# Kernel tuning notes

Hardware: AMD Instinct MI355X
Metric: run time of the kernel (lower is better)

## Reference

```python
import jax, jax.numpy as jnp
import numpy as np

B, T, D, H, F = 4, 2048, 512, 8, 2048
WINDOW = 128
HD = D // H
EPS = 1e-5


def layer_norm(x, g, b):
    mu = jnp.mean(x, axis=-1, keepdims=True)
    var = jnp.mean(jnp.square(x - mu), axis=-1, keepdims=True)
    return (x - mu) * jax.lax.rsqrt(var + EPS) * g + b


def setup_inputs() -> dict:
    key = jax.random.key(0)
    ks = jax.random.split(key, 5)
    s = 0.02
    return {
        "x": jax.random.normal(ks[0], (B, T, D), dtype=jnp.float32),
        "in_proj_w": jax.random.normal(ks[1], (3 * D, D), dtype=jnp.float32) * s,
        "in_proj_b": jnp.zeros((3 * D,), dtype=jnp.float32),
        "out_w": jax.random.normal(ks[2], (D, D), dtype=jnp.float32) * s,
        "out_b": jnp.zeros((D,), dtype=jnp.float32),
        "ln1_g": jnp.ones((D,), dtype=jnp.float32),
        "ln1_b": jnp.zeros((D,), dtype=jnp.float32),
        "ln2_g": jnp.ones((D,), dtype=jnp.float32),
        "ln2_b": jnp.zeros((D,), dtype=jnp.float32),
        "w1": jax.random.normal(ks[3], (F, D), dtype=jnp.float32) * s,
        "b1": jnp.zeros((F,), dtype=jnp.float32),
        "w2": jax.random.normal(ks[4], (D, F), dtype=jnp.float32) * s,
        "b2": jnp.zeros((D,), dtype=jnp.float32),
    }


def reference(x, in_proj_w, in_proj_b, out_w, out_b, ln1_g, ln1_b, ln2_g, ln2_b, w1, b1, w2, b2):
    # pre-norm sliding-window causal self-attention
    x2 = layer_norm(x, ln1_g, ln1_b)
    qkv = x2 @ in_proj_w.T + in_proj_b  # (B,T,3D)
    q, k, v = jnp.split(qkv, 3, axis=-1)
    q = q.reshape(B, T, H, HD)
    k = k.reshape(B, T, H, HD)
    v = v.reshape(B, T, H, HD)
    scale = 1.0 / np.sqrt(HD).astype(np.float32)
    scores = jnp.einsum("bthd,bshd->bhts", q, k) * scale  # dense (B,H,T,T)
    idx = jnp.arange(T)
    i = idx[:, None]
    j = idx[None, :]
    allowed = (j <= i) & (j >= i - WINDOW + 1)  # (T,T) bool, True = attend
    scores = jnp.where(allowed[None, None], scores, -jnp.inf)
    attn = jax.nn.softmax(scores, axis=-1)
    ctx = jnp.einsum("bhts,bshd->bthd", attn, v).reshape(B, T, D)
    attn_out = ctx @ out_w.T + out_b
    x = x + attn_out  # dropout is identity in eval
    # FFN block
    x3 = layer_norm(x, ln2_g, ln2_b)
    h = jax.nn.gelu(x3 @ w1.T + b1, approximate=False)
    x = x + h @ w2.T + b2
    return x
```

## Files before the change

### kernel.cpp

```cpp
#include <hip/hip_runtime.h>
#include <math.h>

constexpr int Bn = 4;
constexpr int Tn = 2048;
constexpr int Dn = 512;
constexpr int Hn = 8;
constexpr int HDn = 64;
constexpr int Fn = 2048;
constexpr int WIN = 128;
constexpr float EPS = 1e-5f;
constexpr int Mrows = Bn * Tn;
constexpr int QKVD = 3 * Dn;

using short8 = __attribute__((ext_vector_type(8))) short;
using f32x4  = __attribute__((ext_vector_type(4))) float;

__device__ __forceinline__ short f2bf(float f) {
    unsigned u = __float_as_uint(f);
    unsigned r = (u + 0x7FFFu + ((u >> 16) & 1u)) >> 16;
    return (short)r;
}

__device__ __forceinline__ float gelu_exact(float v) {
    return 0.5f * v * (1.0f + erff(v * 0.70710678118654752f));
}

__device__ __forceinline__ void async16(const short* g, short* l) {
    __builtin_amdgcn_global_load_lds(
        (const __attribute__((address_space(1))) void*)g,
        (__attribute__((address_space(3))) void*)l,
        16, 0, 0);
}

__global__ __launch_bounds__(256) void cvt_all(const float* __restrict__ s0,
                                               const float* __restrict__ s1,
                                               const float* __restrict__ s2,
                                               const float* __restrict__ s3,
                                               short* __restrict__ d0,
                                               short* __restrict__ d1,
                                               short* __restrict__ d2,
                                               short* __restrict__ d3)
{
    int i = blockIdx.x * 256 + threadIdx.x;
    const float* src; short* dst; int j;
    if (i < 196608)      { src = s0; dst = d0; j = i; }
    else if (i < 262144) { src = s1; dst = d1; j = i - 196608; }
    else if (i < 524288) { src = s2; dst = d2; j = i - 262144; }
    else                 { src = s3; dst = d3; j = i - 524288; }
    float4 v = ((const float4*)src)[j];
    short4 o;
    o.x = f2bf(v.x); o.y = f2bf(v.y); o.z = f2bf(v.z); o.w = f2bf(v.w);
    ((short4*)dst)[j] = o;
}

__global__ __launch_bounds__(64) void ln_kernel(const float* __restrict__ x,
                                                const float* __restrict__ g,
                                                const float* __restrict__ b,
                                                short* __restrict__ y)
{
    int row = blockIdx.x;
    int lane = threadIdx.x;
    const float4* xr = (const float4*)(x + (size_t)row * Dn);
    float4 v0 = xr[lane];
    float4 v1 = xr[lane + 64];
    float s = v0.x + v0.y + v0.z + v0.w + v1.x + v1.y + v1.z + v1.w;
#pragma unroll
    for (int off = 32; off >= 1; off >>= 1) s += __shfl_xor(s, off, 64);
    float mu = s * (1.0f / Dn);
    float d0x = v0.x - mu, d0y = v0.y - mu, d0z = v0.z - mu, d0w = v0.w - mu;
    float d1x = v1.x - mu, d1y = v1.y - mu, d1z = v1.z - mu, d1w = v1.w - mu;
    float q = d0x*d0x + d0y*d0y + d0z*d0z + d0w*d0w
            + d1x*d1x + d1y*d1y + d1z*d1z + d1w*d1w;
#pragma unroll
    for (int off = 32; off >= 1; off >>= 1) q += __shfl_xor(q, off, 64);
    float inv = rsqrtf(q * (1.0f / Dn) + EPS);
    const float4* gr = (const float4*)g;
    const float4* br = (const float4*)b;
    float4 g0 = gr[lane], g1 = gr[lane + 64];
    float4 b0 = br[lane], b1 = br[lane + 64];
    short4 a0, a1;
    a0.x = f2bf(d0x * inv * g0.x + b0.x);
    a0.y = f2bf(d0y * inv * g0.y + b0.y);
    a0.z = f2bf(d0z * inv * g0.z + b0.z);
    a0.w = f2bf(d0w * inv * g0.w + b0.w);
    a1.x = f2bf(d1x * inv * g1.x + b1.x);
    a1.y = f2bf(d1y * inv * g1.y + b1.y);
    a1.z = f2bf(d1z * inv * g1.z + b1.z);
    a1.w = f2bf(d1w * inv * g1.w + b1.w);
    short4* yr = (short4*)(y + (size_t)row * Dn);
    yr[lane] = a0;
    yr[lane + 64] = a1;
}

template <int MODE, int BK>
__global__ __launch_bounds__(256) void gemm_mfma(const short* __restrict__ A,
                                                 const short* __restrict__ Bw,
                                                 const float* __restrict__ bias,
                                                 const float* __restrict__ resid,
                                                 void* __restrict__ Cout,
                                                 short* __restrict__ q_out,
                                                 short* __restrict__ k_out,
                                                 short* __restrict__ v_out,
                                                 int M, int N, int K)
{
    constexpr int NCH = BK / 8;
    constexpr int LGN = (BK == 32) ? 2 : 3;
    constexpr int RPI = 512 / BK;
    constexpr int NI  = 32 / RPI;
    constexpr int BUF = 128 * BK;
    constexpr int KK  = BK / 32;
    __shared__ short SMEM[4 * BUF];
    short* Asb = SMEM;
    short* Bsb = SMEM + 2 * BUF;

    int tid = threadIdx.x;
    int w = tid >> 6, lane = tid & 63;
    int wr = w >> 1, wc = w & 1;
    int nN = N >> 7;
    int bid = blockIdx.x;
    int xcd = bid & 7, sq = bid >> 3;
    int mi = xcd + 8 * (sq / nN);
    int ni = sq % nN;
    int m0 = mi * 128, n0 = ni * 128;
    int quad = lane >> 4, l16 = lane & 15;

    f32x4 zero = {0.f, 0.f, 0.f, 0.f};
    f32x4 acc[4][4];
#pragma unroll
    for (int i = 0; i < 4; ++i)
#pragma unroll
        for (int j = 0; j < 4; ++j) acc[i][j] = zero;

    int rl = lane >> LGN;
    int ch = lane & (NCH - 1);
    const short* Ag[NI];
    const short* Bg[NI];
    int ldsOff[NI];
#pragma unroll
    for (int s = 0; s < NI; ++s) {
        int rowl = w * 32 + s * RPI + rl;
        int csw = (ch ^ ((rowl * BK >> 6) & (NCH - 1))) * 8;
        Ag[s] = A + (size_t)(m0 + rowl) * K + csw;
        Bg[s] = Bw + (size_t)(n0 + rowl) * K + csw;
        ldsOff[s] = (w * 32 + s * RPI) * BK;
    }

    auto stage = [&](int kt, int pp) {
#pragma unroll
        for (int s = 0; s < NI; ++s) {
            async16(Ag[s] + kt, Asb + pp * BUF + ldsOff[s]);
            async16(Bg[s] + kt, Bsb + pp * BUF + ldsOff[s]);
        }
    };

    stage(0, 0);
    int p = 0;
    for (int kt = 0; kt < K; kt += BK) {
        __syncthreads();
        if (kt + BK < K) stage(kt + BK, p ^ 1);
        short8 aF[KK][4], bF[KK][4];
#pragma unroll
        for (int kk = 0; kk < KK; ++kk)
#pragma unroll
            for (int i = 0; i < 4; ++i) {
                int ra = wr * 64 + i * 16 + l16;
                int rb = wc * 64 + i * 16 + l16;
                int cs = ((kk * 4 + quad) ^ ((ra * BK >> 6) & (NCH - 1))) * 8;
                aF[kk][i] = *(const short8*)(Asb + p * BUF + ra * BK + cs);
                bF[kk][i] = *(const short8*)(Bsb + p * BUF + rb * BK + cs);
            }
#pragma unroll
        for (int kk = 0; kk < KK; ++kk)
#pragma unroll
            for (int i = 0; i < 4; ++i)
#pragma unroll
                for (int j = 0; j < 4; ++j)
                    acc[i][j] = __builtin_amdgcn_mfma_f32_16x16x32_bf16(
                        aF[kk][i], bF[kk][j], acc[i][j], 0, 0, 0);
        p ^= 1;
    }

    if constexpr (MODE == 3) {
        __syncthreads();
        short* rp = SMEM + w * 2176;
        int b = m0 >> 11;
        int ncol0 = n0 + wc * 64;
        int sec = ncol0 >> 9;
        int h = (ncol0 & 511) >> 6;
        int bh = b * 8 + h;
        int t0 = (m0 & 2047) + wr * 64;
        if (sec == 2) {
#pragma unroll
            for (int ph = 0; ph < 2; ++ph) {
#pragma unroll
                for (int j = 2 * ph; j < 2 * ph + 2; ++j) {
                    int dl = (j - 2 * ph) * 16 + l16;
                    float bv = bias[ncol0 + j * 16 + l16];
#pragma unroll
                    for (int i = 0; i < 4; ++i)
#pragma unroll
                        for (int r = 0; r < 4; ++r)
                            rp[dl * 68 + i * 16 + quad * 4 + r] = f2bf(acc[i][j][r] + bv);
                }
#pragma unroll
                for (int it = 0; it < 4; ++it) {
                    int row = it * 8 + (lane >> 3);
                    int off = (lane & 7) * 8;
                    *(short8*)(v_out + ((size_t)bh * 64 + 32 * ph + row) * 2048 + t0 + off) =
                        *(const short8*)(rp + row * 68 + off);
                }
            }
        } else {
            short* dst = (sec == 0 ? q_out : k_out);
#pragma unroll
            for (int ph = 0; ph < 2; ++ph) {
#pragma unroll
                for (int i = 2 * ph; i < 2 * ph + 2; ++i) {
                    int tl = (i - 2 * ph) * 16 + quad * 4;
#pragma unroll
                    for (int j = 0; j < 4; ++j) {
                        float bv = bias[ncol0 + j * 16 + l16];
#pragma unroll
                        for (int r = 0; r < 4; ++r)
                            rp[(tl + r) * 68 + j * 16 + l16] = f2bf(acc[i][j][r] + bv);
                    }
                }
#pragma unroll
                for (int it = 0; it < 4; ++it) {
                    int row = it * 8 + (lane >> 3);
                    int off = (lane & 7) * 8;
                    *(short8*)(dst + ((size_t)bh * 2048 + t0 + 32 * ph + row) * 64 + off) =
                        *(const short8*)(rp + row * 68 + off);
                }
            }
        }
        return;
    }

    if constexpr (MODE == 2) {
        __syncthreads();
        short* rp = SMEM + w * 2176;
        short* Cb = (short*)Cout;
#pragma unroll
        for (int ph = 0; ph < 2; ++ph) {
#pragma unroll
            for (int i = 2 * ph; i < 2 * ph + 2; ++i) {
                int ml = (i - 2 * ph) * 16 + quad * 4;
#pragma unroll
                for (int j = 0; j < 4; ++j) {
                    float bv = bias[n0 + wc * 64 + j * 16 + l16];
#pragma unroll
                    for (int r = 0; r < 4; ++r)
                        rp[(ml + r) * 68 + j * 16 + l16] =
                            f2bf(gelu_exact(acc[i][j][r] + bv));
                }
            }
#pragma unroll
            for (int it = 0; it < 4; ++it) {
                int row = it * 8 + (lane >> 3);
                int off = (lane & 7) * 8;
                *(short8*)(Cb + (size_t)(m0 + wr * 64 + 32 * ph + row) * N
                              + n0 + wc * 64 + off) =
                    *(const short8*)(rp + row * 68 + off);
            }
        }
        return;
    }

    float* Cf = (float*)Cout;
#pragma unroll
    for (int j = 0; j < 4; ++j) {
        int n = n0 + wc * 64 + j * 16 + l16;
        float bv = bias[n];
#pragma unroll
        for (int i = 0; i < 4; ++i) {
            int mbase = m0 + wr * 64 + i * 16 + quad * 4;
#pragma unroll
            for (int r = 0; r < 4; ++r) {
                size_t idx = (size_t)(mbase + r) * N + n;
                Cf[idx] = acc[i][j][r] + bv + resid[idx];
            }
        }
    }
}

constexpr int QS = 72;
constexpr int VS = 200;

__global__ __launch_bounds__(256) void attn_mfma(const short* __restrict__ Qg,
                                                 const short* __restrict__ Kg,
                                                 const short* __restrict__ Vtg,
                                                 short* __restrict__ ctx)
{
    __shared__ short Qs[64 * QS];
    __shared__ short Ks[192 * QS];
    __shared__ short Vt[64 * VS];
    int tid = threadIdx.x;
    int w = tid >> 6, lane = tid & 63, quad = lane >> 4, l16 = lane & 15;
    int blk = blockIdx.x;
    int q0 = (blk & 31) << 6;
    int bh = blk >> 5;
    int kbase = q0 - 128;

    {
        const short* src = Qg + ((size_t)bh * 2048 + q0) * 64;
        for (int c = tid; c < 512; c += 256) {
            int row = c >> 3, off = (c & 7) * 8;
            *(short8*)(Qs + row * QS + off) = *(const short8*)(src + row * 64 + off);
        }
    }
    {
        const short* base = Kg + (size_t)bh * 2048 * 64;
        for (int c = tid; c < 1536; c += 256) {
            int row = c >> 3, off = (c & 7) * 8;
            int srow = kbase + row; srow = srow < 0 ? 0 : srow;
            *(short8*)(Ks + row * QS + off) = *(const short8*)(base + (size_t)srow * 64 + off);
        }
    }
    {
        const short* base = Vtg + (size_t)bh * 64 * 2048;
        for (int c = tid; c < 1536; c += 256) {
            int row = c / 24, cc = c - row * 24;
            int off = cc * 8;
            int scol = kbase + off; scol = scol < 0 ? 0 : scol;
            *(short8*)(Vt + row * VS + off) = *(const short8*)(base + (size_t)row * 2048 + scol);
        }
    }
    __syncthreads();

    short8 aF0 = *(const short8*)(Qs + (w * 16 + l16) * QS + quad * 8);
    short8 aF1 = *(const short8*)(Qs + (w * 16 + l16) * QS + 32 + quad * 8);
    f32x4 S[12];
    f32x4 zero = {0.f, 0.f, 0.f, 0.f};
#pragma unroll
    for (int t = 0; t < 12; ++t) S[t] = zero;
#pragma unroll
    for (int t = 0; t < 12; ++t) {
        short8 b0 = *(const short8*)(Ks + (t * 16 + l16) * QS + quad * 8);
        short8 b1 = *(const short8*)(Ks + (t * 16 + l16) * QS + 32 + quad * 8);
        S[t] = __builtin_amdgcn_mfma_f32_16x16x32_bf16(aF0, b0, S[t], 0, 0, 0);
        S[t] = __builtin_amdgcn_mfma_f32_16x16x32_bf16(aF1, b1, S[t], 0, 0, 0);
    }

    int i0 = w * 16 + quad * 4;
    float mrow[4] = {-INFINITY, -INFINITY, -INFINITY, -INFINITY};
#pragma unroll
    for (int t = 0; t < 12; ++t) {
        int jl = t * 16 + l16;
        int kg = kbase + jl;
#pragma unroll
        for (int r = 0; r < 4; ++r) {
            int dj = jl - (i0 + r);
            bool ok = (dj >= 1) && (dj <= 128) && (kg >= 0);
            float s = ok ? S[t][r] * 0.125f : -INFINITY;
            S[t][r] = s;
            mrow[r] = fmaxf(mrow[r], s);
        }
    }
#pragma unroll
    for (int off = 8; off >= 1; off >>= 1)
#pragma unroll
        for (int r = 0; r < 4; ++r)
            mrow[r] = fmaxf(mrow[r], __shfl_xor(mrow[r], off, 64));
    float sum[4] = {0.f, 0.f, 0.f, 0.f};
#pragma unroll
    for (int t = 0; t < 12; ++t)
#pragma unroll
        for (int r = 0; r < 4; ++r) {
            float p = __expf(S[t][r] - mrow[r]);
            S[t][r] = p;
            sum[r] += p;
        }
#pragma unroll
    for (int off = 8; off >= 1; off >>= 1)
#pragma unroll
        for (int r = 0; r < 4; ++r)
            sum[r] += __shfl_xor(sum[r], off, 64);
    float inv[4];
#pragma unroll
    for (int r = 0; r < 4; ++r) inv[r] = 1.0f / sum[r];

    __syncthreads();
    short* Ps = Ks;
#pragma unroll
    for (int t = 0; t < 12; ++t)
#pragma unroll
        for (int r = 0; r < 4; ++r)
            Ps[(w * 16 + quad * 4 + r) * VS + t * 16 + l16] = f2bf(S[t][r]);

    f32x4 O[4];
#pragma unroll
    for (int tN = 0; tN < 4; ++tN) O[tN] = zero;
#pragma unroll
    for (int s = 0; s < 6; ++s) {
        short8 aP = *(const short8*)(Ps + (w * 16 + l16) * VS + s * 32 + quad * 8);
#pragma unroll
        for (int tN = 0; tN < 4; ++tN) {
            short8 bV = *(const short8*)(Vt + (tN * 16 + l16) * VS + s * 32 + quad * 8);
            O[tN] = __builtin_amdgcn_mfma_f32_16x16x32_bf16(aP, bV, O[tN], 0, 0, 0);
        }
    }

    int b = bh >> 3, h = bh & 7;
#pragma unroll
    for (int tN = 0; tN < 4; ++tN)
#pragma unroll
        for (int r = 0; r < 4; ++r) {
            int trow = q0 + w * 16 + quad * 4 + r;
            ctx[((size_t)(b * 2048 + trow)) * 512 + h * 64 + tN * 16 + l16] =
                f2bf(O[tN][r] * inv[r]);
        }
}

extern "C" void kernel_launch(void* const* d_in, const int* in_sizes, int n_in,
                              void* d_out, int out_size, void* d_ws, size_t ws_size,
                              hipStream_t stream)
{
    const float* x         = (const float*)d_in[0];
    const float* in_proj_w = (const float*)d_in[1];
    const float* in_proj_b = (const float*)d_in[2];
    const float* out_w     = (const float*)d_in[3];
    const float* out_b     = (const float*)d_in[4];
    const float* ln1_g     = (const float*)d_in[5];
    const float* ln1_b     = (const float*)d_in[6];
    const float* ln2_g     = (const float*)d_in[7];
    const float* ln2_b     = (const float*)d_in[8];
    const float* w1        = (const float*)d_in[9];
    const float* b1        = (const float*)d_in[10];
    const float* w2        = (const float*)d_in[11];
    const float* b2        = (const float*)d_in[12];
    float* out = (float*)d_out;

    char* ws = (char*)d_ws;
    short* attnQ = (short*)ws;
    short* attnK = (short*)(ws + (size_t)8 * 1024 * 1024);
    short* attnV = (short*)(ws + (size_t)16 * 1024 * 1024);
    short* hbuf  = (short*)ws;
    short* regB  = (short*)(ws + (size_t)32 * 1024 * 1024);
    short* wq  = (short*)(ws + (size_t)40 * 1024 * 1024);
    short* wo  = wq + (size_t)QKVD * Dn;
    short* w1b = wo + (size_t)Dn * Dn;
    short* w2b = w1b + (size_t)Fn * Dn;

    cvt_all<<<3072, 256, 0, stream>>>(in_proj_w, out_w, w1, w2, wq, wo, w1b, w2b);

    ln_kernel<<<Mrows, 64, 0, stream>>>(x, ln1_g, ln1_b, regB);
    gemm_mfma<3, 32><<<(Mrows / 128) * (QKVD / 128), 256, 0, stream>>>(
        regB, wq, in_proj_b, nullptr, nullptr, attnQ, attnK, attnV, Mrows, QKVD, Dn);
    attn_mfma<<<Bn * Hn * (Tn / 64), 256, 0, stream>>>(attnQ, attnK, attnV, regB);
    gemm_mfma<1, 64><<<(Mrows / 128) * (Dn / 128), 256, 0, stream>>>(
        regB, wo, out_b, x, out, nullptr, nullptr, nullptr, Mrows, Dn, Dn);
    ln_kernel<<<Mrows, 64, 0, stream>>>(out, ln2_g, ln2_b, regB);
    gemm_mfma<2, 32><<<(Mrows / 128) * (Fn / 128), 256, 0, stream>>>(
        regB, w1b, b1, nullptr, hbuf, nullptr, nullptr, nullptr, Mrows, Fn, Dn);
    gemm_mfma<1, 64><<<(Mrows / 128) * (Dn / 128), 256, 0, stream>>>(
        hbuf, w2b, b2, out, out, nullptr, nullptr, nullptr, Mrows, Dn, Fn);
}
```

Baseline: 223.3 us.

## Switch GEMM to triple-buffered LDS pipeline with partial vmcnt waits

Replaces the double-buffered GEMM main loop with a three-stage LDS ring at fixed BK=32. The next tile is issued before waiting, and an explicit s_waitcnt vmcnt(4) plus a raw s_barrier lets one stage of loads stay in flight, so the former __syncthreads drains no longer stall the loop. LDS fragment offsets are also precomputed outside the loop. The out-projection and FFN2 GEMMs lose their BK=64 tiles, so they now run more barriers per K step. Relying on the vmcnt count to order the async copies is fragile if the load count ever changes.

```diff
diff --git a/kernel.cpp b/kernel.cpp
--- a/kernel.cpp
+++ b/kernel.cpp
@@ -92,7 +92,7 @@
     yr[lane + 64] = a1;
 }
 
-template <int MODE, int BK>
+template <int MODE>
 __global__ __launch_bounds__(256) void gemm_mfma(const short* __restrict__ A,
                                                  const short* __restrict__ Bw,
                                                  const float* __restrict__ bias,
@@ -103,16 +103,9 @@
                                                  short* __restrict__ v_out,
                                                  int M, int N, int K)
 {
-    constexpr int NCH = BK / 8;
-    constexpr int LGN = (BK == 32) ? 2 : 3;
-    constexpr int RPI = 512 / BK;
-    constexpr int NI  = 32 / RPI;
+    constexpr int BK = 32;
     constexpr int BUF = 128 * BK;
-    constexpr int KK  = BK / 32;
-    __shared__ short SMEM[4 * BUF];
-    short* Asb = SMEM;
-    short* Bsb = SMEM + 2 * BUF;
-
+    __shared__ short SMEM[6 * BUF];
     int tid = threadIdx.x;
     int w = tid >> 6, lane = tid & 63;
     int wr = w >> 1, wc = w & 1;
@@ -131,53 +124,64 @@
 #pragma unroll
         for (int j = 0; j < 4; ++j) acc[i][j] = zero;
 
-    int rl = lane >> LGN;
-    int ch = lane & (NCH - 1);
-    const short* Ag[NI];
-    const short* Bg[NI];
-    int ldsOff[NI];
-#pragma unroll
-    for (int s = 0; s < NI; ++s) {
-        int rowl = w * 32 + s * RPI + rl;
-        int csw = (ch ^ ((rowl * BK >> 6) & (NCH - 1))) * 8;
+    int rl = lane >> 2;
+    int ch = lane & 3;
+    const short* Ag[2];
+    const short* Bg[2];
+    int ldsOff[2];
+#pragma unroll
+    for (int s = 0; s < 2; ++s) {
+        int rowl = w * 32 + s * 16 + rl;
+        int csw = (ch ^ ((rowl >> 1) & 3)) * 8;
         Ag[s] = A + (size_t)(m0 + rowl) * K + csw;
         Bg[s] = Bw + (size_t)(n0 + rowl) * K + csw;
-        ldsOff[s] = (w * 32 + s * RPI) * BK;
-    }
-
-    auto stage = [&](int kt, int pp) {
-#pragma unroll
-        for (int s = 0; s < NI; ++s) {
-            async16(Ag[s] + kt, Asb + pp * BUF + ldsOff[s]);
-            async16(Bg[s] + kt, Bsb + pp * BUF + ldsOff[s]);
+        ldsOff[s] = (w * 32 + s * 16) * BK;
+    }
+
+    auto stage = [&](int kt, int qb) {
+        short* Ab = SMEM + qb * (2 * BUF);
+        short* Bb = Ab + BUF;
+#pragma unroll
+        for (int s = 0; s < 2; ++s) {
+            async16(Ag[s] + kt, Ab + ldsOff[s]);
+            async16(Bg[s] + kt, Bb + ldsOff[s]);
         }
     };
 
+    int aoff[4], boff[4];
+#pragma unroll
+    for (int i = 0; i < 4; ++i) {
+        int ra = wr * 64 + i * 16 + l16;
+        int rb = wc * 64 + i * 16 + l16;
+        aoff[i] = ra * BK + (quad ^ ((ra >> 1) & 3)) * 8;
+        boff[i] = rb * BK + (quad ^ ((rb >> 1) & 3)) * 8;
+    }
+
     stage(0, 0);
-    int p = 0;
+    int q = 0, qn = 1;
     for (int kt = 0; kt < K; kt += BK) {
-        __syncthreads();
-        if (kt + BK < K) stage(kt + BK, p ^ 1);
-        short8 aF[KK][4], bF[KK][4];
-#pragma unroll
-        for (int kk = 0; kk < KK; ++kk)
-#pragma unroll
-            for (int i = 0; i < 4; ++i) {
-                int ra = wr * 64 + i * 16 + l16;
-                int rb = wc * 64 + i * 16 + l16;
-                int cs = ((kk * 4 + quad) ^ ((ra * BK >> 6) & (NCH - 1))) * 8;
-                aF[kk][i] = *(const short8*)(Asb + p * BUF + ra * BK + cs);
-                bF[kk][i] = *(const short8*)(Bsb + p * BUF + rb * BK + cs);
-            }
-#pragma unroll
-        for (int kk = 0; kk < KK; ++kk)
-#pragma unroll
-            for (int i = 0; i < 4; ++i)
-#pragma unroll
-                for (int j = 0; j < 4; ++j)
-                    acc[i][j] = __builtin_amdgcn_mfma_f32_16x16x32_bf16(
-                        aF[kk][i], bF[kk][j], acc[i][j], 0, 0, 0);
-        p ^= 1;
+        if (kt + BK < K) {
+            stage(kt + BK, qn);
+            asm volatile("s_waitcnt vmcnt(4)" ::: "memory");
+        } else {
+            asm volatile("s_waitcnt vmcnt(0)" ::: "memory");
+        }
+        asm volatile("s_barrier" ::: "memory");
+        const short* Ab = SMEM + q * (2 * BUF);
+        const short* Bb = Ab + BUF;
+        short8 aF[4], bF[4];
+#pragma unroll
+        for (int i = 0; i < 4; ++i) {
+            aF[i] = *(const short8*)(Ab + aoff[i]);
+            bF[i] = *(const short8*)(Bb + boff[i]);
+        }
+#pragma unroll
+        for (int i = 0; i < 4; ++i)
+#pragma unroll
+            for (int j = 0; j < 4; ++j)
+                acc[i][j] = __builtin_amdgcn_mfma_f32_16x16x32_bf16(
+                    aF[i], bF[j], acc[i][j], 0, 0, 0);
+        q = qn; qn = (qn == 2) ? 0 : qn + 1;
     }
 
     if constexpr (MODE == 3) {
@@ -445,14 +449,14 @@
     cvt_all<<<3072, 256, 0, stream>>>(in_proj_w, out_w, w1, w2, wq, wo, w1b, w2b);
 
     ln_kernel<<<Mrows, 64, 0, stream>>>(x, ln1_g, ln1_b, regB);
-    gemm_mfma<3, 32><<<(Mrows / 128) * (QKVD / 128), 256, 0, stream>>>(
+    gemm_mfma<3><<<(Mrows / 128) * (QKVD / 128), 256, 0, stream>>>(
         regB, wq, in_proj_b, nullptr, nullptr, attnQ, attnK, attnV, Mrows, QKVD, Dn);
     attn_mfma<<<Bn * Hn * (Tn / 64), 256, 0, stream>>>(attnQ, attnK, attnV, regB);
-    gemm_mfma<1, 64><<<(Mrows / 128) * (Dn / 128), 256, 0, stream>>>(
+    gemm_mfma<1><<<(Mrows / 128) * (Dn / 128), 256, 0, stream>>>(
         regB, wo, out_b, x, out, nullptr, nullptr, nullptr, Mrows, Dn, Dn);
     ln_kernel<<<Mrows, 64, 0, stream>>>(out, ln2_g, ln2_b, regB);
-    gemm_mfma<2, 32><<<(Mrows / 128) * (Fn / 128), 256, 0, stream>>>(
+    gemm_mfma<2><<<(Mrows / 128) * (Fn / 128), 256, 0, stream>>>(
         regB, w1b, b1, nullptr, hbuf, nullptr, nullptr, nullptr, Mrows, Fn, Dn);
-    gemm_mfma<1, 64><<<(Mrows / 128) * (Dn / 128), 256, 0, stream>>>(
+    gemm_mfma<1><<<(Mrows / 128) * (Dn / 128), 256, 0, stream>>>(
         hbuf, w2b, b2, out, out, nullptr, nullptr, nullptr, Mrows, Dn, Fn);
 }
```

Result: no change. 226.6 us (+1.5%).
